# Kernel tuning notes

Hardware: AMD Instinct MI355X
Metric: run time of the kernel (lower is better)

## Reference

```python
import jax, jax.numpy as jnp
import numpy as np
from jax import lax

T, X, H = 16384, 256, 1024
A_SCALE, A_IDENT = 0.1, 0.9


def setup_inputs() -> dict:
    key = jax.random.key(0)
    k1, k2, k3 = jax.random.split(key, 3)
    x_seq = jax.random.normal(k1, (T, X), dtype=jnp.float32)
    h0 = jnp.zeros((H,), dtype=jnp.float32)
    # orthogonal-like init for A_raw (QR of a gaussian), lecun_normal for B
    g = jax.random.normal(k2, (H, H), dtype=jnp.float32)
    A_raw, _ = jnp.linalg.qr(g)
    B = jax.random.normal(k3, (H, X), dtype=jnp.float32) * (1.0 / np.sqrt(X))
    c = jnp.zeros((H,), dtype=jnp.float32)
    return {"x_seq": x_seq, "h0": h0, "A_raw": A_raw, "B": B, "c": c}


def reference(x_seq, h0, A_raw, B, c):
    # A = a_identity * I + a_scale * A_raw  (computed in setup(), a parameter transform)
    A = A_IDENT * jnp.eye(H, dtype=x_seq.dtype) + A_SCALE * A_raw
    # Precompute input projections for all timesteps as one GEMM: (T,H)
    Bx_c = x_seq @ B.T + c  # B @ x_t + c for every t

    def step(h, bx_t):
        h_new = jnp.tanh(A @ h + bx_t)
        return h_new, h_new

    _, h_all = lax.scan(step, h0, Bx_c)
    return h_all  # (T, H)
```

## Files before the change

kernel.cpp:

```cpp
#include <hip/hip_runtime.h>
#include <cstdint>

#define T_LEN 16384
#define X_DIM 256
#define H_DIM 1024
#define NREP  8
#define SLOT_U32 1280
#define REP_U32  (2 * SLOT_U32)
#define FLAG_OFF (NREP * REP_U32)

typedef unsigned int u32;
typedef u32   u32x4 __attribute__((ext_vector_type(4)));
typedef float f32x4 __attribute__((ext_vector_type(4)));

__device__ __forceinline__ void coh_store4(u32* p, u32x4 v) {
  asm volatile("global_store_dwordx4 %0, %1, off sc0 sc1" :: "v"(p), "v"(v) : "memory");
}
__device__ __forceinline__ void coh_store1(u32* p, u32 v) {
  asm volatile("global_store_dword %0, %1, off sc0 sc1" :: "v"(p), "v"(v) : "memory");
}
__device__ __forceinline__ u32 coh_load1(const u32* p) {
  u32 v;
  asm volatile("global_load_dword %0, %1, off sc0 sc1\n\ts_waitcnt vmcnt(0)"
               : "=v"(v) : "v"(p) : "memory");
  return v;
}
__device__ __forceinline__ void poll_group(const u32* p, u32x4& a, u32x4& b,
                                           u32x4& c, u32x4& d) {
  asm volatile(
      "global_load_dwordx4 %0, %4, off sc0 sc1\n\t"
      "global_load_dwordx4 %1, %4, off offset:16 sc0 sc1\n\t"
      "global_load_dwordx4 %2, %4, off offset:32 sc0 sc1\n\t"
      "global_load_dwordx4 %3, %4, off offset:48 sc0 sc1\n\t"
      "s_waitcnt vmcnt(0)"
      : "=&v"(a), "=&v"(b), "=&v"(c), "=&v"(d) : "v"(p) : "memory");
}

__device__ __forceinline__ float fast_tanh(float x) {
  x = fminf(9.0f, fmaxf(-9.0f, x));
  const float e = __builtin_amdgcn_exp2f(x * 2.8853900817779268f);
  return (e - 1.0f) * __builtin_amdgcn_rcpf(e + 1.0f);
}


__global__ void hinit(const float* __restrict__ h0, u32* __restrict__ ws) {
  const int i = threadIdx.x;
  const f32x4 h = *(const f32x4*)(h0 + i * 4);
  u32x4 v;
  v.x = __float_as_uint(h[0]) & ~3u;
  v.y = __float_as_uint(h[1]) & ~3u;
  v.z = __float_as_uint(h[2]) & ~3u;
  v.w = __float_as_uint(h[3]) & ~3u;
  const int c = i * 4;
  const int idx = 20 * (c >> 4) + (c & 15);
#pragma unroll
  for (int rep = 0; rep < NREP; ++rep)
    coh_store4(ws + (size_t)rep * REP_U32 + idx, v);
  if (i < 2) coh_store1(ws + FLAG_OFF + i, 0u);
}

__global__ __launch_bounds__(256) void gemm_bx(const float* __restrict__ x,
                                               const float* __restrict__ Bm,
                                               const float* __restrict__ c,
                                               float* __restrict__ out) {
  __shared__ float xs[64][68];
  __shared__ float bs[64][68];

  const int tid = threadIdx.x;
  const int t0  = blockIdx.x * 64;
  const int h0  = blockIdx.y * 64;
  const int lr  = tid >> 4;
  const int lc  = tid & 15;

  float acc[4][4] = {};

  for (int kb = 0; kb < X_DIM; kb += 64) {
    const int kk  = (tid & 15) * 4;
    const int tt0 = tid >> 4;
#pragma unroll
    for (int i = 0; i < 4; ++i) {
      const int tt = tt0 + i * 16;
      const f32x4 xv = *(const f32x4*)(x  + (size_t)(t0 + tt) * X_DIM + kb + kk);
      const f32x4 bv = *(const f32x4*)(Bm + (size_t)(h0 + tt) * X_DIM + kb + kk);
#pragma unroll
      for (int q = 0; q < 4; ++q) {
        xs[kk + q][tt] = xv[q];
        bs[kk + q][tt] = bv[q];
      }
    }
    __syncthreads();

#pragma unroll 8
    for (int k = 0; k < 64; ++k) {
      const f32x4 xv = *(const f32x4*)&xs[k][lr * 4];
      const f32x4 bv = *(const f32x4*)&bs[k][lc * 4];
#pragma unroll
      for (int i = 0; i < 4; ++i)
#pragma unroll
        for (int j = 0; j < 4; ++j)
          acc[i][j] = fmaf(xv[i], bv[j], acc[i][j]);
    }
    __syncthreads();
  }

  const f32x4 cv = *(const f32x4*)(c + h0 + lc * 4);
#pragma unroll
  for (int i = 0; i < 4; ++i) {
    f32x4 o;
#pragma unroll
    for (int j = 0; j < 4; ++j) o[j] = acc[i][j] + cv[j];
    *(f32x4*)(out + (size_t)(t0 + lr * 4 + i) * H_DIM + h0 + lc * 4) = o;
  }
}

__global__ __launch_bounds__(256) void rnn_scan(const float* __restrict__ A_raw,
                                                float* __restrict__ out,
                                                u32* __restrict__ ws) {
  const int tid = threadIdx.x;

  if (blockIdx.x >= 64) {
    const u32* flag = ws + FLAG_OFF;
    float f0 = 0.f, f1 = 0.f, f2 = 0.f, f3 = 0.f;
    float f4 = 0.f, f5 = 0.f, f6 = 0.f, f7 = 0.f;
    const float m = 1.0000001f, ad = 1e-9f;
    for (int outer = 0; outer < 32768; ++outer) {
      if (coh_load1(flag) != 0u) break;
      for (int i = 0; i < 256; ++i) {
        f0 = fmaf(f0, m, ad); f1 = fmaf(f1, m, ad);
        f2 = fmaf(f2, m, ad); f3 = fmaf(f3, m, ad);
        f4 = fmaf(f4, m, ad); f5 = fmaf(f5, m, ad);
        f6 = fmaf(f6, m, ad); f7 = fmaf(f7, m, ad);
      }
    }
    if (f0 + f1 + f2 + f3 + f4 + f5 + f6 + f7 == 123456.789f && tid == 0)
      coh_store1(ws + FLAG_OFF + 1, 1u);
    return;
  }

  const int lane    = tid & 63;
  const int wv      = tid >> 6;
  const int wg      = blockIdx.x;
  const int gw      = wg * 4 + wv;
  const int rowbase = gw * 4;
  const int r       = lane & 3;
  const int s       = lane >> 2;
  const int row     = rowbase + r;

  __shared__ u32 hs[2 * SLOT_U32 + 2];
  volatile u32* vtags = hs + 2 * SLOT_U32;
  if (tid == 0) { vtags[0] = 0xFFFFFFFFu; vtags[1] = 0xFFFFFFFFu; }
  __syncthreads();

  float a[4][16];
#pragma unroll
  for (int seg = 0; seg < 4; ++seg) {
#pragma unroll
    for (int k4 = 0; k4 < 4; ++k4) {
      const f32x4 v = *(const f32x4*)(A_raw + (size_t)row * H_DIM +
                                      seg * 256 + s * 16 + k4 * 4);
#pragma unroll
      for (int q = 0; q < 4; ++q) {
        const int col = seg * 256 + s * 16 + k4 * 4 + q;
        a[seg][k4 * 4 + q] = 0.1f * v[q] + (col == row ? 0.9f : 0.0f);
      }
    }
  }

  u32* hbuf   = ws;
  u32* my_rep = hbuf + (size_t)(wg & (NREP - 1)) * REP_U32;

  float bx_val = out[(size_t)0 * H_DIM + row];

  for (int t = 0; t < T_LEN; ++t) {
    u32* lbuf = hs + (t & 1) * SLOT_U32;

    if (wv == 0) {
      const u32 tag = (u32)(t & 3);
      const u32* p  = my_rep + (size_t)(t & 1) * SLOT_U32 + 20 * lane;
      u32x4 hA, hB, hC, hD;
      for (;;) {
        poll_group(p, hA, hB, hC, hD);
        const u32 m = (hA.x ^ tag) | (hA.y ^ tag) | (hA.z ^ tag) | (hA.w ^ tag)
                    | (hB.x ^ tag) | (hB.y ^ tag) | (hB.z ^ tag) | (hB.w ^ tag)
                    | (hC.x ^ tag) | (hC.y ^ tag) | (hC.z ^ tag) | (hC.w ^ tag)
                    | (hD.x ^ tag) | (hD.y ^ tag) | (hD.z ^ tag) | (hD.w ^ tag);
        if ((m & 3u) == 0u) break;
      }
      u32* w = lbuf + 20 * lane;
      *(u32x4*)(w)      = hA;
      *(u32x4*)(w + 4)  = hB;
      *(u32x4*)(w + 8)  = hC;
      *(u32x4*)(w + 12) = hD;
      asm volatile("s_waitcnt lgkmcnt(0)" ::: "memory");
      if (lane == 0) vtags[t & 1] = (u32)t;
    } else {
      while (vtags[t & 1] != (u32)t) {  }
    }
    asm volatile("" ::: "memory");

    const int tn1 = (t + 1 < T_LEN) ? t + 1 : t;
    const float bx_next = out[(size_t)tn1 * H_DIM + row];

    const u32* rb = lbuf + 20 * s;
    float ac0 = 0.f, ac1 = 0.f, ac2 = 0.f, ac3 = 0.f;
#pragma unroll
    for (int seg = 0; seg < 4; ++seg) {
      const f32x4 f0 = __builtin_bit_cast(f32x4, *(const u32x4*)(rb + 320 * seg));
      const f32x4 f1 = __builtin_bit_cast(f32x4, *(const u32x4*)(rb + 320 * seg + 4));
      const f32x4 f2 = __builtin_bit_cast(f32x4, *(const u32x4*)(rb + 320 * seg + 8));
      const f32x4 f3 = __builtin_bit_cast(f32x4, *(const u32x4*)(rb + 320 * seg + 12));
#pragma unroll
      for (int j = 0; j < 4; ++j) {
        ac0 = fmaf(a[seg][j],      f0[j], ac0);
        ac1 = fmaf(a[seg][4 + j],  f1[j], ac1);
        ac2 = fmaf(a[seg][8 + j],  f2[j], ac2);
        ac3 = fmaf(a[seg][12 + j], f3[j], ac3);
      }
    }
    float acc = (ac0 + ac1) + (ac2 + ac3);
#pragma unroll
    for (int d = 4; d < 64; d <<= 1) acc += __shfl_xor(acc, d, 64);

    const float v = fast_tanh(acc + bx_val);
    bx_val = bx_next;

    const u32 nt = (u32)((t + 1) & 3);
    if (lane < 4 * NREP) {
      const int rep = lane >> 2;
      u32* dst = hbuf + (size_t)rep * REP_U32 + (size_t)((t + 1) & 1) * SLOT_U32
               + 20 * (rowbase >> 4) + (rowbase & 15) + r;
      coh_store1(dst, (__float_as_uint(v) & ~3u) | nt);
    } else if (lane < 4 * NREP + 4) {
      out[(size_t)t * H_DIM + rowbase + r] = v;
    }
  }

  if (wg == 0 && tid == 0) coh_store1(ws + FLAG_OFF, 1u);
}

extern "C" void kernel_launch(void* const* d_in, const int* in_sizes, int n_in,
                              void* d_out, int out_size, void* d_ws, size_t ws_size,
                              hipStream_t stream) {
  const float* x    = (const float*)d_in[0];
  const float* h0   = (const float*)d_in[1];
  const float* Araw = (const float*)d_in[2];
  const float* B    = (const float*)d_in[3];
  const float* c    = (const float*)d_in[4];
  float* out = (float*)d_out;
  u32* ws    = (u32*)d_ws;

  hinit<<<1, 256, 0, stream>>>(h0, ws);
  dim3 g(T_LEN / 64, H_DIM / 64);
  gemm_bx<<<g, 256, 0, stream>>>(x, B, c, out);
  rnn_scan<<<256, 256, 0, stream>>>(Araw, out, ws);
}
```

Measured before the change: 25.42 ms.

## Poll global state per wavefront directly, dropping LDS staging and intra-block sync

```diff
diff --git a/kernel.cpp b/kernel.cpp
--- a/kernel.cpp
+++ b/kernel.cpp
@@ -5,7 +5,7 @@
 #define X_DIM 256
 #define H_DIM 1024
 #define NREP  8
-#define SLOT_U32 1280
+#define SLOT_U32 1024
 #define REP_U32  (2 * SLOT_U32)
 #define FLAG_OFF (NREP * REP_U32)
 
@@ -42,6 +42,20 @@
   return (e - 1.0f) * __builtin_amdgcn_rcpf(e + 1.0f);
 }
 
+template <int CTRL>
+__device__ __forceinline__ float ror_add(float x) {
+  const int y = __builtin_amdgcn_update_dpp(0, __float_as_int(x), CTRL, 0xF, 0xF, false);
+  return x + __int_as_float(y);
+}
+__device__ __forceinline__ float redux64(float x) {
+  x = ror_add<0x121>(x);
+  x = ror_add<0x122>(x);
+  x = ror_add<0x124>(x);
+  x = ror_add<0x128>(x);
+  x += __shfl_xor(x, 16, 64);
+  x += __shfl_xor(x, 32, 64);
+  return x;
+}
 
 __global__ void hinit(const float* __restrict__ h0, u32* __restrict__ ws) {
   const int i = threadIdx.x;
@@ -51,8 +65,7 @@
   v.y = __float_as_uint(h[1]) & ~3u;
   v.z = __float_as_uint(h[2]) & ~3u;
   v.w = __float_as_uint(h[3]) & ~3u;
-  const int c = i * 4;
-  const int idx = 20 * (c >> 4) + (c & 15);
+  const int idx = i * 4;
 #pragma unroll
   for (int rep = 0; rep < NREP; ++rep)
     coh_store4(ws + (size_t)rep * REP_U32 + idx, v);
@@ -143,99 +156,103 @@
   const int gw      = wg * 4 + wv;
   const int rowbase = gw * 4;
   const int r       = lane & 3;
-  const int s       = lane >> 2;
   const int row     = rowbase + r;
 
-  __shared__ u32 hs[2 * SLOT_U32 + 2];
-  volatile u32* vtags = hs + 2 * SLOT_U32;
-  if (tid == 0) { vtags[0] = 0xFFFFFFFFu; vtags[1] = 0xFFFFFFFFu; }
-  __syncthreads();
-
   float a[4][16];
 #pragma unroll
-  for (int seg = 0; seg < 4; ++seg) {
+  for (int rr = 0; rr < 4; ++rr) {
 #pragma unroll
     for (int k4 = 0; k4 < 4; ++k4) {
-      const f32x4 v = *(const f32x4*)(A_raw + (size_t)row * H_DIM +
-                                      seg * 256 + s * 16 + k4 * 4);
+      const f32x4 v = *(const f32x4*)(A_raw + (size_t)(rowbase + rr) * H_DIM +
+                                      lane * 16 + k4 * 4);
 #pragma unroll
       for (int q = 0; q < 4; ++q) {
-        const int col = seg * 256 + s * 16 + k4 * 4 + q;
-        a[seg][k4 * 4 + q] = 0.1f * v[q] + (col == row ? 0.9f : 0.0f);
+        const int col = lane * 16 + k4 * 4 + q;
+        a[rr][k4 * 4 + q] = 0.1f * v[q] + (col == rowbase + rr ? 0.9f : 0.0f);
       }
     }
   }
 
-  u32* hbuf   = ws;
-  u32* my_rep = hbuf + (size_t)(wg & (NREP - 1)) * REP_U32;
+  u32* hbuf = ws;
+  const u32* ppoll0 = hbuf + (size_t)(gw & (NREP - 1)) * REP_U32 + 16 * lane;
+  u32* pub = hbuf + (size_t)(lane >> 2) * REP_U32 + rowbase + r;
 
   float bx_val = out[(size_t)0 * H_DIM + row];
+  float bx_n1  = out[(size_t)1 * H_DIM + row];
+
+  int  dead    = 1 << 20;
+  bool timeout = false;
 
   for (int t = 0; t < T_LEN; ++t) {
-    u32* lbuf = hs + (t & 1) * SLOT_U32;
-
-    if (wv == 0) {
-      const u32 tag = (u32)(t & 3);
-      const u32* p  = my_rep + (size_t)(t & 1) * SLOT_U32 + 20 * lane;
-      u32x4 hA, hB, hC, hD;
-      for (;;) {
-        poll_group(p, hA, hB, hC, hD);
-        const u32 m = (hA.x ^ tag) | (hA.y ^ tag) | (hA.z ^ tag) | (hA.w ^ tag)
-                    | (hB.x ^ tag) | (hB.y ^ tag) | (hB.z ^ tag) | (hB.w ^ tag)
-                    | (hC.x ^ tag) | (hC.y ^ tag) | (hC.z ^ tag) | (hC.w ^ tag)
-                    | (hD.x ^ tag) | (hD.y ^ tag) | (hD.z ^ tag) | (hD.w ^ tag);
-        if ((m & 3u) == 0u) break;
-      }
-      u32* w = lbuf + 20 * lane;
-      *(u32x4*)(w)      = hA;
-      *(u32x4*)(w + 4)  = hB;
-      *(u32x4*)(w + 8)  = hC;
-      *(u32x4*)(w + 12) = hD;
-      asm volatile("s_waitcnt lgkmcnt(0)" ::: "memory");
-      if (lane == 0) vtags[t & 1] = (u32)t;
-    } else {
-      while (vtags[t & 1] != (u32)t) {  }
-    }
-    asm volatile("" ::: "memory");
-
-    const int tn1 = (t + 1 < T_LEN) ? t + 1 : t;
-    const float bx_next = out[(size_t)tn1 * H_DIM + row];
-
-    const u32* rb = lbuf + 20 * s;
+    const u32 tag = (u32)(t & 3);
+    const u32* p  = ppoll0 + (t & 1) * SLOT_U32;
+    u32x4 hA, hB, hC, hD;
+    for (;;) {
+      poll_group(p, hA, hB, hC, hD);
+      const u32 m = (hA.x ^ tag) | (hA.y ^ tag) | (hA.z ^ tag) | (hA.w ^ tag)
+                  | (hB.x ^ tag) | (hB.y ^ tag) | (hB.z ^ tag) | (hB.w ^ tag)
+                  | (hC.x ^ tag) | (hC.y ^ tag) | (hC.z ^ tag) | (hC.w ^ tag)
+                  | (hD.x ^ tag) | (hD.y ^ tag) | (hD.z ^ tag) | (hD.w ^ tag);
+      if ((m & 3u) == 0u) break;
+      if (--dead == 0) { timeout = true; break; }
+    }
+    if (__any(timeout)) {
+      if (lane == 0) coh_store1(ws + FLAG_OFF, 1u);
+      return;
+    }
+
+    const int tn2 = (t + 2 < T_LEN) ? t + 2 : t;
+    const float bx_n2 = out[(size_t)tn2 * H_DIM + row];
+
+    const f32x4 f0 = __builtin_bit_cast(f32x4, hA);
+    const f32x4 f1 = __builtin_bit_cast(f32x4, hB);
+    const f32x4 f2 = __builtin_bit_cast(f32x4, hC);
+    const f32x4 f3 = __builtin_bit_cast(f32x4, hD);
     float ac0 = 0.f, ac1 = 0.f, ac2 = 0.f, ac3 = 0.f;
 #pragma unroll
-    for (int seg = 0; seg < 4; ++seg) {
-      const f32x4 f0 = __builtin_bit_cast(f32x4, *(const u32x4*)(rb + 320 * seg));
-      const f32x4 f1 = __builtin_bit_cast(f32x4, *(const u32x4*)(rb + 320 * seg + 4));
-      const f32x4 f2 = __builtin_bit_cast(f32x4, *(const u32x4*)(rb + 320 * seg + 8));
-      const f32x4 f3 = __builtin_bit_cast(f32x4, *(const u32x4*)(rb + 320 * seg + 12));
-#pragma unroll
-      for (int j = 0; j < 4; ++j) {
-        ac0 = fmaf(a[seg][j],      f0[j], ac0);
-        ac1 = fmaf(a[seg][4 + j],  f1[j], ac1);
-        ac2 = fmaf(a[seg][8 + j],  f2[j], ac2);
-        ac3 = fmaf(a[seg][12 + j], f3[j], ac3);
-      }
-    }
-    float acc = (ac0 + ac1) + (ac2 + ac3);
-#pragma unroll
-    for (int d = 4; d < 64; d <<= 1) acc += __shfl_xor(acc, d, 64);
-
-    const float v = fast_tanh(acc + bx_val);
-    bx_val = bx_next;
+    for (int j = 0; j < 4; ++j) {
+      ac0 = fmaf(a[0][j], f0[j], ac0); ac1 = fmaf(a[1][j], f0[j], ac1);
+      ac2 = fmaf(a[2][j], f0[j], ac2); ac3 = fmaf(a[3][j], f0[j], ac3);
+    }
+#pragma unroll
+    for (int j = 0; j < 4; ++j) {
+      ac0 = fmaf(a[0][4 + j], f1[j], ac0); ac1 = fmaf(a[1][4 + j], f1[j], ac1);
+      ac2 = fmaf(a[2][4 + j], f1[j], ac2); ac3 = fmaf(a[3][4 + j], f1[j], ac3);
+    }
+#pragma unroll
+    for (int j = 0; j < 4; ++j) {
+      ac0 = fmaf(a[0][8 + j], f2[j], ac0); ac1 = fmaf(a[1][8 + j], f2[j], ac1);
+      ac2 = fmaf(a[2][8 + j], f2[j], ac2); ac3 = fmaf(a[3][8 + j], f2[j], ac3);
+    }
+#pragma unroll
+    for (int j = 0; j < 4; ++j) {
+      ac0 = fmaf(a[0][12 + j], f3[j], ac0); ac1 = fmaf(a[1][12 + j], f3[j], ac1);
+      ac2 = fmaf(a[2][12 + j], f3[j], ac2); ac3 = fmaf(a[3][12 + j], f3[j], ac3);
+    }
+
+    ac0 = redux64(ac0);
+    ac1 = redux64(ac1);
+    ac2 = redux64(ac2);
+    ac3 = redux64(ac3);
+
+    float accr = ac0;
+    if (r == 1) accr = ac1;
+    if (r == 2) accr = ac2;
+    if (r == 3) accr = ac3;
+    const float v = fast_tanh(accr + bx_val);
+    bx_val = bx_n1;
+    bx_n1  = bx_n2;
 
     const u32 nt = (u32)((t + 1) & 3);
     if (lane < 4 * NREP) {
-      const int rep = lane >> 2;
-      u32* dst = hbuf + (size_t)rep * REP_U32 + (size_t)((t + 1) & 1) * SLOT_U32
-               + 20 * (rowbase >> 4) + (rowbase & 15) + r;
-      coh_store1(dst, (__float_as_uint(v) & ~3u) | nt);
+      coh_store1(pub + (size_t)((t + 1) & 1) * SLOT_U32,
+                 (__float_as_uint(v) & ~3u) | nt);
     } else if (lane < 4 * NREP + 4) {
-      out[(size_t)t * H_DIM + rowbase + r] = v;
-    }
-  }
-
-  if (wg == 0 && tid == 0) coh_store1(ws + FLAG_OFF, 1u);
+      out[(size_t)t * H_DIM + row] = v;
+    }
+  }
+
+  if (gw == 0 && lane == 0) coh_store1(ws + FLAG_OFF, 1u);
 }
 
 extern "C" void kernel_launch(void* const* d_in, const int* in_sizes, int n_in,
```

Result: faster. 22.25 ms (-12.5%).
